# Kernel optimization log

Measured on AMD Instinct MI355X. Metric: run time of the kernel, lower is better.

## Reference

```python
import jax, jax.numpy as jnp
import numpy as np

DIM = 1024
B, K = 8192, 16


def setup_inputs() -> dict:
    key = jax.random.key(0)
    ks = jax.random.split(key, 7)
    # xavier_uniform bound for square [C,C]: sqrt(6/(C+C))
    bq = float(np.sqrt(6.0 / (DIM + DIM)))
    ba_bound = float(np.sqrt(6.0 / (DIM + 1)))
    return {
        "query": jax.random.normal(ks[0], (B, DIM), dtype=jnp.float32),
        "key": jax.random.normal(ks[1], (B, K, DIM), dtype=jnp.float32),
        "value": jax.random.normal(ks[2], (B, K, DIM), dtype=jnp.float32),
        "Wq": jax.random.uniform(ks[3], (DIM, DIM), jnp.float32, -bq, bq),
        "Wk": jax.random.uniform(ks[4], (DIM, DIM), jnp.float32, -bq, bq),
        "Wa": jax.random.uniform(ks[5], (1, DIM), jnp.float32, -ba_bound, ba_bound),
        "ba": jnp.ones((1,), dtype=jnp.float32),
    }


def reference(query, key, value, Wq, Wk, Wa, ba):
    # query: [B, C]; key/value: [B, K, C]
    C = query.shape[-1]
    res = query
    q = query[:, None, :]                       # [B, 1, C]
    k = jnp.concatenate([q, key], axis=1)       # [B, K+1, C] (query prepended)
    v = jnp.concatenate([q, value], axis=1)     # [B, K+1, C]
    qp = q @ Wq.T                               # [B, 1, C]
    kp = k @ Wk.T                               # [B, K+1, C]
    scale = 1.0 / jnp.sqrt(jnp.asarray(C, dtype=jnp.float32))
    scores = jnp.einsum('bqc,bkc->bqk', qp, kp) * scale   # [B, 1, K+1]
    attn_w = jax.nn.softmax(scores, axis=-1)
    attn = jnp.einsum('bqk,bkc->bqc', attn_w, v)[:, 0, :]  # [B, C]
    alpha = jax.nn.sigmoid(res @ Wa.T + ba)     # [B, 1]
    out = res + alpha * attn                    # gated residual
    # F.normalize(p=2, dim=-1, eps=1e-12)
    norm = jnp.linalg.norm(out, axis=-1, keepdims=True)
    return out / jnp.maximum(norm, 1e-12)
```

## Files before the change

kernel.cpp:

```cpp
#include <hip/hip_runtime.h>
#include <hip/hip_bf16.h>

#define DIM   1024
#define BATCH 8192
#define KV    16

typedef __attribute__((ext_vector_type(4))) float f32x4;
typedef __attribute__((ext_vector_type(8))) short short8;

static __device__ __forceinline__ unsigned short f2bf(float x) {
  return __builtin_bit_cast(unsigned short, __float2bfloat16(x));
}
static __device__ __forceinline__ float bf2f(unsigned short x) {
  return __bfloat162float(__builtin_bit_cast(__hip_bfloat16, x));
}
static __device__ __forceinline__ float dot4(f32x4 a, f32x4 b) {
  return a.x * b.x + a.y * b.y + a.z * b.z + a.w * b.w;
}

static __device__ __forceinline__ void gl_lds16(const unsigned short* g, unsigned short* l) {
  __builtin_amdgcn_global_load_lds(
      (const __attribute__((address_space(1))) void*)g,
      (__attribute__((address_space(3))) void*)l, 16, 0, 0);
}

__global__ __launch_bounds__(256) void convert_q(const f32x4* __restrict__ in,
                                                 ushort4* __restrict__ out, int n4) {
  int i = blockIdx.x * blockDim.x + threadIdx.x;
  int stride = gridDim.x * blockDim.x;
  for (; i < n4; i += stride) {
    f32x4 f = in[i];
    ushort4 o;
    o.x = f2bf(f.x); o.y = f2bf(f.y); o.z = f2bf(f.z); o.w = f2bf(f.w);
    out[i] = o;
  }
}

__global__ __launch_bounds__(256) void transpose_w(const float* __restrict__ Wq,
                                                   const float* __restrict__ Wk,
                                                   unsigned short* __restrict__ WqT,
                                                   unsigned short* __restrict__ WkT) {
  __shared__ float tile[32][33];
  const float* src = blockIdx.z ? Wk : Wq;
  unsigned short* dst = blockIdx.z ? WkT : WqT;
  int x = blockIdx.x * 32 + threadIdx.x;
  int y0 = blockIdx.y * 32;
  #pragma unroll
  for (int i = threadIdx.y; i < 32; i += 8)
    tile[i][threadIdx.x] = src[(size_t)(y0 + i) * DIM + x];
  __syncthreads();
  int x2 = blockIdx.y * 32 + threadIdx.x;
  int y2 = blockIdx.x * 32;
  #pragma unroll
  for (int i = threadIdx.y; i < 32; i += 8)
    dst[(size_t)(y2 + i) * DIM + x2] = f2bf(tile[threadIdx.x][i]);
}

__global__ __launch_bounds__(256) void gemm_nt64(const unsigned short* __restrict__ A,
                                                 const unsigned short* __restrict__ B,
                                                 unsigned short* __restrict__ C,
                                                 int N, int K) {
  __shared__ __align__(16) unsigned short As[64 * 32];
  __shared__ __align__(16) unsigned short Bs[64 * 32];
  const int tid = threadIdx.x;
  const int lane = tid & 63;
  const int wave = tid >> 6;
  const int wr = wave >> 1, wc = wave & 1;
  const size_t bm = (size_t)blockIdx.x * 64;
  const size_t bn = (size_t)blockIdx.y * 64;

  f32x4 acc[2][2];
  #pragma unroll
  for (int m = 0; m < 2; ++m)
    #pragma unroll
    for (int n = 0; n < 2; ++n)
      acc[m][n] = (f32x4){0.f, 0.f, 0.f, 0.f};

  const int r0 = tid >> 2;
  const int cc = (tid & 3) * 8;
  const int kg = lane >> 4;
  const int rowf = lane & 15;

  for (int kt = 0; kt < K; kt += 32) {
    gl_lds16(A + (bm + r0) * K + kt + cc, As + tid * 8);
    gl_lds16(B + (bn + r0) * K + kt + cc, Bs + tid * 8);
    __syncthreads();
    short8 af[2], bfr[2];
    #pragma unroll
    for (int m = 0; m < 2; ++m)
      af[m] = *(const short8*)(As + ((wr * 32 + m * 16 + rowf) * 32 + kg * 8));
    #pragma unroll
    for (int n = 0; n < 2; ++n)
      bfr[n] = *(const short8*)(Bs + ((wc * 32 + n * 16 + rowf) * 32 + kg * 8));
    #pragma unroll
    for (int m = 0; m < 2; ++m)
      #pragma unroll
      for (int n = 0; n < 2; ++n)
        acc[m][n] = __builtin_amdgcn_mfma_f32_16x16x32_bf16(af[m], bfr[n], acc[m][n], 0, 0, 0);
    __syncthreads();
  }

  const int rq = (lane >> 4) * 4;
  const int colf = lane & 15;
  #pragma unroll
  for (int m = 0; m < 2; ++m)
    #pragma unroll
    for (int n = 0; n < 2; ++n)
      #pragma unroll
      for (int i = 0; i < 4; ++i)
        C[(bm + wr * 32 + m * 16 + rq + i) * N + bn + wc * 32 + n * 16 + colf] =
            f2bf(acc[m][n][i]);
}

__global__ __launch_bounds__(256) void gemm_u(const unsigned short* __restrict__ A,
                                              const unsigned short* __restrict__ B,
                                              unsigned short* __restrict__ C,
                                              int K, int ntN, int ldc) {
  const int cpx = gridDim.x >> 3;
  const int wg = (blockIdx.x & 7) * cpx + (blockIdx.x >> 3);
  const size_t bm = (size_t)(wg / ntN) * 128;
  const size_t bn = (size_t)(wg % ntN) * 128;

  __shared__ __align__(16) unsigned short As[128 * 32];
  __shared__ __align__(16) unsigned short Bs[128 * 32];
  const int tid = threadIdx.x;
  const int lane = tid & 63;
  const int wave = tid >> 6;
  const int wr = wave >> 1, wc = wave & 1;

  f32x4 acc[4][4];
  #pragma unroll
  for (int m = 0; m < 4; ++m)
    #pragma unroll
    for (int n = 0; n < 4; ++n)
      acc[m][n] = (f32x4){0.f, 0.f, 0.f, 0.f};

  const int r0 = tid >> 2;
  const int r1 = 64 + (tid >> 2);
  const int cc = (tid & 3) * 8;
  const int kg = lane >> 4;
  const int rowf = lane & 15;

  for (int kt = 0; kt < K; kt += 32) {
    gl_lds16(A + (bm + r0) * K + kt + cc, As + tid * 8);
    gl_lds16(A + (bm + r1) * K + kt + cc, As + 2048 + tid * 8);
    gl_lds16(B + (bn + r0) * K + kt + cc, Bs + tid * 8);
    gl_lds16(B + (bn + r1) * K + kt + cc, Bs + 2048 + tid * 8);
    __syncthreads();
    short8 af[4], bfr[4];
    #pragma unroll
    for (int m = 0; m < 4; ++m)
      af[m] = *(const short8*)(As + ((wr * 64 + m * 16 + rowf) * 32 + kg * 8));
    #pragma unroll
    for (int n = 0; n < 4; ++n)
      bfr[n] = *(const short8*)(Bs + ((wc * 64 + n * 16 + rowf) * 32 + kg * 8));
    #pragma unroll
    for (int m = 0; m < 4; ++m)
      #pragma unroll
      for (int n = 0; n < 4; ++n)
        acc[m][n] = __builtin_amdgcn_mfma_f32_16x16x32_bf16(af[m], bfr[n], acc[m][n], 0, 0, 0);
    __syncthreads();
  }

  const int rq = (lane >> 4) * 4;
  const int colf = lane & 15;
  #pragma unroll
  for (int m = 0; m < 4; ++m)
    #pragma unroll
    for (int n = 0; n < 4; ++n)
      #pragma unroll
      for (int i = 0; i < 4; ++i) {
        size_t row = bm + wr * 64 + m * 16 + rq + i;
        size_t col = bn + wc * 64 + n * 16 + colf;
        C[row * (size_t)ldc + col] = f2bf(acc[m][n][i]);
      }
}

__global__ __launch_bounds__(256) void epilogue(const float* __restrict__ query,
                                                const float* __restrict__ key,
                                                const float* __restrict__ value,
                                                const float* __restrict__ Wa,
                                                const float* __restrict__ ba,
                                                const unsigned short* __restrict__ u,
                                                float* __restrict__ out) {
  const int b = blockIdx.x;
  const int tid = threadIdx.x;
  const int lane = tid & 63, wave = tid >> 6;
  const f32x4* q4 = (const f32x4*)(query + (size_t)b * DIM);
  const f32x4* k4 = (const f32x4*)(key + (size_t)b * KV * DIM);
  const f32x4* v4 = (const f32x4*)(value + (size_t)b * KV * DIM);

  f32x4 qv = q4[tid];
  ushort4 ub = ((const ushort4*)(u + (size_t)b * 2048))[tid];
  f32x4 uv;
  uv.x = bf2f(ub.x); uv.y = bf2f(ub.y); uv.z = bf2f(ub.z); uv.w = bf2f(ub.w);
  f32x4 wv = ((const f32x4*)Wa)[tid];

  float s[17];
  s[0] = dot4(qv, uv);
  float ad = dot4(qv, wv);
  #pragma unroll
  for (int j = 1; j <= 16; ++j) {
    f32x4 kv = __builtin_nontemporal_load(k4 + (j - 1) * 256 + tid);
    s[j] = dot4(uv, kv);
  }

  f32x4 vv[16];
  #pragma unroll
  for (int j = 0; j < 16; ++j)
    vv[j] = __builtin_nontemporal_load(v4 + j * 256 + tid);

  #pragma unroll
  for (int m = 32; m >= 1; m >>= 1) {
    #pragma unroll
    for (int j = 0; j < 17; ++j) s[j] += __shfl_xor(s[j], m);
    ad += __shfl_xor(ad, m);
  }
  __shared__ float red[4][18];
  if (lane == 0) {
    #pragma unroll
    for (int j = 0; j < 17; ++j) red[wave][j] = s[j];
    red[wave][17] = ad;
  }
  __syncthreads();

  float wt[17];
  float mx = -1e30f;
  #pragma unroll
  for (int j = 0; j < 17; ++j) {
    float t = (red[0][j] + red[1][j] + red[2][j] + red[3][j]) * 0.03125f;
    wt[j] = t;
    mx = fmaxf(mx, t);
  }
  float den = 0.f;
  #pragma unroll
  for (int j = 0; j < 17; ++j) {
    wt[j] = expf(wt[j] - mx);
    den += wt[j];
  }
  float adt = red[0][17] + red[1][17] + red[2][17] + red[3][17] + ba[0];
  float alpha = 1.0f / (1.0f + expf(-adt));
  float am = alpha / den;

  f32x4 acc = qv * wt[0];
  #pragma unroll
  for (int j = 1; j <= 16; ++j) acc += vv[j - 1] * wt[j];
  f32x4 t = qv + acc * am;

  float ssp = dot4(t, t);
  #pragma unroll
  for (int m = 32; m >= 1; m >>= 1) ssp += __shfl_xor(ssp, m);
  __shared__ float red2[4];
  if (lane == 0) red2[wave] = ssp;
  __syncthreads();
  float nrm = sqrtf(red2[0] + red2[1] + red2[2] + red2[3]);
  float inv = 1.0f / fmaxf(nrm, 1e-12f);

  ((f32x4*)(out + (size_t)b * DIM))[tid] = t * inv;
}

extern "C" void kernel_launch(void* const* d_in, const int* in_sizes, int n_in,
                              void* d_out, int out_size, void* d_ws, size_t ws_size,
                              hipStream_t stream) {
  const float* query = (const float*)d_in[0];
  const float* key   = (const float*)d_in[1];
  const float* value = (const float*)d_in[2];
  const float* Wq    = (const float*)d_in[3];
  const float* Wk    = (const float*)d_in[4];
  const float* Wa    = (const float*)d_in[5];
  const float* ba    = (const float*)d_in[6];

  unsigned short* qbf = (unsigned short*)d_ws;
  unsigned short* WqT = qbf + (size_t)BATCH * DIM;
  unsigned short* WkT = WqT + (size_t)DIM * DIM;
  unsigned short* Mt  = WkT + (size_t)DIM * DIM;
  unsigned short* ubf = (unsigned short*)d_out;

  convert_q<<<2048, 256, 0, stream>>>((const f32x4*)query, (ushort4*)qbf, BATCH * DIM / 4);
  transpose_w<<<dim3(32, 32, 2), dim3(32, 8), 0, stream>>>(Wq, Wk, WqT, WkT);
  gemm_nt64<<<dim3(16, 16), 256, 0, stream>>>(WkT, WqT, Mt, DIM, DIM);
  gemm_u<<<512, 256, 0, stream>>>(qbf, Mt, ubf, DIM, DIM / 128, 2048);
  epilogue<<<BATCH, 256, 0, stream>>>(query, key, value, Wa, ba, ubf, (float*)d_out);
}
```

Baseline: 245.6 us.

## Merge prep kernels, widen gemm_u K-tile, read bf16 query in epilogue

```diff
diff --git a/kernel.cpp b/kernel.cpp
--- a/kernel.cpp
+++ b/kernel.cpp
@@ -24,36 +24,42 @@
       (__attribute__((address_space(3))) void*)l, 16, 0, 0);
 }
 
-__global__ __launch_bounds__(256) void convert_q(const f32x4* __restrict__ in,
-                                                 ushort4* __restrict__ out, int n4) {
-  int i = blockIdx.x * blockDim.x + threadIdx.x;
-  int stride = gridDim.x * blockDim.x;
-  for (; i < n4; i += stride) {
-    f32x4 f = in[i];
-    ushort4 o;
-    o.x = f2bf(f.x); o.y = f2bf(f.y); o.z = f2bf(f.z); o.w = f2bf(f.w);
-    out[i] = o;
-  }
-}
-
-__global__ __launch_bounds__(256) void transpose_w(const float* __restrict__ Wq,
-                                                   const float* __restrict__ Wk,
-                                                   unsigned short* __restrict__ WqT,
-                                                   unsigned short* __restrict__ WkT) {
-  __shared__ float tile[32][33];
-  const float* src = blockIdx.z ? Wk : Wq;
-  unsigned short* dst = blockIdx.z ? WkT : WqT;
-  int x = blockIdx.x * 32 + threadIdx.x;
-  int y0 = blockIdx.y * 32;
-  #pragma unroll
-  for (int i = threadIdx.y; i < 32; i += 8)
-    tile[i][threadIdx.x] = src[(size_t)(y0 + i) * DIM + x];
-  __syncthreads();
-  int x2 = blockIdx.y * 32 + threadIdx.x;
-  int y2 = blockIdx.x * 32;
-  #pragma unroll
-  for (int i = threadIdx.y; i < 32; i += 8)
-    dst[(size_t)(y2 + i) * DIM + x2] = f2bf(tile[threadIdx.x][i]);
+__global__ __launch_bounds__(256) void prep(const float* __restrict__ query,
+                                            unsigned short* __restrict__ qbf,
+                                            const float* __restrict__ Wq,
+                                            const float* __restrict__ Wk,
+                                            unsigned short* __restrict__ WqT,
+                                            unsigned short* __restrict__ WkT) {
+  if (blockIdx.z == 2) {
+    int bid = blockIdx.y * 32 + blockIdx.x;
+    int i = bid * 256 + threadIdx.x;
+    const f32x4* in = (const f32x4*)query;
+    ushort4* out = (ushort4*)qbf;
+    #pragma unroll
+    for (int r = 0; r < 8; ++r) {
+      int idx = i + r * 262144;
+      f32x4 f = in[idx];
+      ushort4 o;
+      o.x = f2bf(f.x); o.y = f2bf(f.y); o.z = f2bf(f.z); o.w = f2bf(f.w);
+      out[idx] = o;
+    }
+  } else {
+    __shared__ float tile[32][33];
+    const float* src = blockIdx.z ? Wk : Wq;
+    unsigned short* dst = blockIdx.z ? WkT : WqT;
+    int tx = threadIdx.x & 31, ty = threadIdx.x >> 5;
+    int x = blockIdx.x * 32 + tx;
+    int y0 = blockIdx.y * 32;
+    #pragma unroll
+    for (int i = ty; i < 32; i += 8)
+      tile[i][tx] = src[(size_t)(y0 + i) * DIM + x];
+    __syncthreads();
+    int x2 = blockIdx.y * 32 + tx;
+    int y2 = blockIdx.x * 32;
+    #pragma unroll
+    for (int i = ty; i < 32; i += 8)
+      dst[(size_t)(y2 + i) * DIM + x2] = f2bf(tile[tx][i]);
+  }
 }
 
 __global__ __launch_bounds__(256) void gemm_nt64(const unsigned short* __restrict__ A,
@@ -115,14 +121,15 @@
 __global__ __launch_bounds__(256) void gemm_u(const unsigned short* __restrict__ A,
                                               const unsigned short* __restrict__ B,
                                               unsigned short* __restrict__ C,
-                                              int K, int ntN, int ldc) {
+                                              int ntN, int ldc) {
+  __shared__ __align__(16) unsigned short As[128 * 64];
+  __shared__ __align__(16) unsigned short Bs[128 * 64];
+
   const int cpx = gridDim.x >> 3;
   const int wg = (blockIdx.x & 7) * cpx + (blockIdx.x >> 3);
   const size_t bm = (size_t)(wg / ntN) * 128;
   const size_t bn = (size_t)(wg % ntN) * 128;
 
-  __shared__ __align__(16) unsigned short As[128 * 32];
-  __shared__ __align__(16) unsigned short Bs[128 * 32];
   const int tid = threadIdx.x;
   const int lane = tid & 63;
   const int wave = tid >> 6;
@@ -135,30 +142,34 @@
     for (int n = 0; n < 4; ++n)
       acc[m][n] = (f32x4){0.f, 0.f, 0.f, 0.f};
 
-  const int r0 = tid >> 2;
-  const int r1 = 64 + (tid >> 2);
-  const int cc = (tid & 3) * 8;
   const int kg = lane >> 4;
   const int rowf = lane & 15;
 
-  for (int kt = 0; kt < K; kt += 32) {
-    gl_lds16(A + (bm + r0) * K + kt + cc, As + tid * 8);
-    gl_lds16(A + (bm + r1) * K + kt + cc, As + 2048 + tid * 8);
-    gl_lds16(B + (bn + r0) * K + kt + cc, Bs + tid * 8);
-    gl_lds16(B + (bn + r1) * K + kt + cc, Bs + 2048 + tid * 8);
-    __syncthreads();
-    short8 af[4], bfr[4];
-    #pragma unroll
-    for (int m = 0; m < 4; ++m)
-      af[m] = *(const short8*)(As + ((wr * 64 + m * 16 + rowf) * 32 + kg * 8));
-    #pragma unroll
-    for (int n = 0; n < 4; ++n)
-      bfr[n] = *(const short8*)(Bs + ((wc * 64 + n * 16 + rowf) * 32 + kg * 8));
-    #pragma unroll
-    for (int m = 0; m < 4; ++m)
+  for (int kt = 0; kt < DIM; kt += 64) {
+    #pragma unroll
+    for (int it = 0; it < 4; ++it) {
+      int c = it * 256 + tid;
+      int r = c >> 3;
+      int ko = (c & 7) * 8;
+      gl_lds16(A + (bm + r) * DIM + kt + ko, As + c * 8);
+      gl_lds16(B + (bn + r) * DIM + kt + ko, Bs + c * 8);
+    }
+    __syncthreads();
+    #pragma unroll
+    for (int ks = 0; ks < 2; ++ks) {
+      short8 af[4], bfr[4];
+      #pragma unroll
+      for (int m = 0; m < 4; ++m)
+        af[m] = *(const short8*)(As + (wr * 64 + m * 16 + rowf) * 64 + ks * 32 + kg * 8);
       #pragma unroll
       for (int n = 0; n < 4; ++n)
-        acc[m][n] = __builtin_amdgcn_mfma_f32_16x16x32_bf16(af[m], bfr[n], acc[m][n], 0, 0, 0);
+        bfr[n] = *(const short8*)(Bs + (wc * 64 + n * 16 + rowf) * 64 + ks * 32 + kg * 8);
+      #pragma unroll
+      for (int m = 0; m < 4; ++m)
+        #pragma unroll
+        for (int n = 0; n < 4; ++n)
+          acc[m][n] = __builtin_amdgcn_mfma_f32_16x16x32_bf16(af[m], bfr[n], acc[m][n], 0, 0, 0);
+    }
     __syncthreads();
   }
 
@@ -176,7 +187,7 @@
       }
 }
 
-__global__ __launch_bounds__(256) void epilogue(const float* __restrict__ query,
+__global__ __launch_bounds__(256) void epilogue(const unsigned short* __restrict__ qbf,
                                                 const float* __restrict__ key,
                                                 const float* __restrict__ value,
                                                 const float* __restrict__ Wa,
@@ -186,11 +197,12 @@
   const int b = blockIdx.x;
   const int tid = threadIdx.x;
   const int lane = tid & 63, wave = tid >> 6;
-  const f32x4* q4 = (const f32x4*)(query + (size_t)b * DIM);
   const f32x4* k4 = (const f32x4*)(key + (size_t)b * KV * DIM);
   const f32x4* v4 = (const f32x4*)(value + (size_t)b * KV * DIM);
 
-  f32x4 qv = q4[tid];
+  ushort4 qb4 = *(const ushort4*)(qbf + (size_t)b * DIM + tid * 4);
+  f32x4 qv;
+  qv.x = bf2f(qb4.x); qv.y = bf2f(qb4.y); qv.z = bf2f(qb4.z); qv.w = bf2f(qb4.w);
   ushort4 ub = ((const ushort4*)(u + (size_t)b * 2048))[tid];
   f32x4 uv;
   uv.x = bf2f(ub.x); uv.y = bf2f(ub.y); uv.z = bf2f(ub.z); uv.w = bf2f(ub.w);
@@ -256,7 +268,7 @@
   float nrm = sqrtf(red2[0] + red2[1] + red2[2] + red2[3]);
   float inv = 1.0f / fmaxf(nrm, 1e-12f);
 
-  ((f32x4*)(out + (size_t)b * DIM))[tid] = t * inv;
+  __builtin_nontemporal_store(t * inv, (f32x4*)(out + (size_t)b * DIM) + tid);
 }
 
 extern "C" void kernel_launch(void* const* d_in, const int* in_sizes, int n_in,
@@ -276,9 +288,8 @@
   unsigned short* Mt  = WkT + (size_t)DIM * DIM;
   unsigned short* ubf = (unsigned short*)d_out;
 
-  convert_q<<<2048, 256, 0, stream>>>((const f32x4*)query, (ushort4*)qbf, BATCH * DIM / 4);
-  transpose_w<<<dim3(32, 32, 2), dim3(32, 8), 0, stream>>>(Wq, Wk, WqT, WkT);
+  prep<<<dim3(32, 32, 3), 256, 0, stream>>>(query, qbf, Wq, Wk, WqT, WkT);
   gemm_nt64<<<dim3(16, 16), 256, 0, stream>>>(WkT, WqT, Mt, DIM, DIM);
-  gemm_u<<<512, 256, 0, stream>>>(qbf, Mt, ubf, DIM, DIM / 128, 2048);
-  epilogue<<<BATCH, 256, 0, stream>>>(query, key, value, Wa, ba, ubf, (float*)d_out);
-}
+  gemm_u<<<512, 256, 0, stream>>>(qbf, Mt, ubf, DIM / 128, 2048);
+  epilogue<<<BATCH, 256, 0, stream>>>(qbf, key, value, Wa, ba, ubf, (float*)d_out);
+}
```

After: 246.2 us. Within noise of the previous version (+0.2%).
